# Optimization experiments

Hardware: AMD Instinct MI355X
Metric: run time of the kernel (lower is better)

The kernel has to match this reference:

```python
import jax, jax.numpy as jnp
import numpy as np

N_QUBITS = 4
N_LAYERS = 2
BATCH = 2097152  # 2**21

# All gates (RY, CNOT) are real-valued and the initial state |0..0> is real,
# so the whole simulation stays in float32; <Z> is then real automatically
# (matching the .real taken in the torch module).

def _apply_ry(state, theta, q):
    """Apply RY(theta) on qubit q. state: (B,2,2,2,2); theta: scalar or (B,)."""
    s = jnp.moveaxis(state, 1 + q, -1)           # qubit axis -> last
    half = theta * 0.5
    c, sn = jnp.cos(half), jnp.sin(half)
    a, bamp = s[..., 0], s[..., 1]               # (B,2,2,2)
    # broadcast per-sample angles over remaining qubit axes
    c = jnp.reshape(c, c.shape + (1,) * (a.ndim - c.ndim))
    sn = jnp.reshape(sn, sn.shape + (1,) * (a.ndim - sn.ndim))
    new = jnp.stack([c * a - sn * bamp, sn * a + c * bamp], axis=-1)
    return jnp.moveaxis(new, -1, 1 + q)


def _apply_cnot(state, ctrl, tgt):
    """CNOT(ctrl -> tgt). Swap target amplitudes where control bit is 1."""
    s = jnp.moveaxis(state, (1 + ctrl, 1 + tgt), (-2, -1))
    s = jnp.stack([s[..., 0, :], s[..., 1, ::-1]], axis=-2)
    return jnp.moveaxis(s, (-2, -1), (1 + ctrl, 1 + tgt))


def _circuit(x, weights):
    """x: (B, n_qubits) angles; weights: (n_layers, n_qubits). Returns (B, n_qubits) <Z_i>."""
    B = x.shape[0]
    state = jnp.zeros((B,) + (2,) * N_QUBITS, dtype=x.dtype)
    state = state.at[(slice(None),) + (0,) * N_QUBITS].set(1.0)  # |0000>
    for i in range(N_QUBITS):
        state = _apply_ry(state, x[:, i], i)
    for l in range(N_LAYERS):
        for i in range(N_QUBITS):
            state = _apply_cnot(state, i, (i + 1) % N_QUBITS)
        for i in range(N_QUBITS):
            state = _apply_ry(state, weights[l, i], i)
    p = state * state                             # probabilities (real state)
    zs = []
    for i in range(N_QUBITS):
        pm = jnp.moveaxis(p, 1 + i, -1)
        zs.append((pm[..., 0] - pm[..., 1]).sum(axis=(1, 2, 3)))
    return jnp.stack(zs, axis=-1)


def setup_inputs() -> dict:
    key = jax.random.key(0)
    k1, k2, k3, k4 = jax.random.split(key, 4)
    return {
        "x": jax.random.normal(k1, (BATCH, N_QUBITS), dtype=jnp.float32),
        "weights": jax.random.normal(k2, (N_LAYERS, N_QUBITS), dtype=jnp.float32),
        "W": jax.random.normal(k3, (2, N_QUBITS), dtype=jnp.float32) / np.sqrt(N_QUBITS),
        "b": jax.random.normal(k4, (2,), dtype=jnp.float32) * 0.01,
    }


def reference(x, weights, W, b):
    features = _circuit(x, weights)               # (B, 4)
    return features @ W.T + b                     # (B, 2)
```

## Files before the change

### kernel.cpp

```cpp
#include <hip/hip_runtime.h>


template<int BIT>
__device__ __forceinline__ void apply_ry(float (&a)[16], float c, float s) {
#pragma unroll
    for (int i = 0; i < 16; ++i) {
        if ((i & BIT) == 0) {
            float a0 = a[i];
            float a1 = a[i | BIT];
            a[i]       = __builtin_fmaf(c, a0, -(s * a1));
            a[i | BIT] = __builtin_fmaf(s, a0,  (c * a1));
        }
    }
}

template<int CBIT, int TBIT>
__device__ __forceinline__ void apply_cnot(float (&a)[16]) {
#pragma unroll
    for (int i = 0; i < 16; ++i) {
        if ((i & CBIT) != 0 && (i & TBIT) == 0) {
            float t = a[i];
            a[i] = a[i | TBIT];
            a[i | TBIT] = t;
        }
    }
}

__global__ __launch_bounds__(256) void qsim_kernel(
    const float4* __restrict__ x4,
    const float*  __restrict__ wts,
    const float*  __restrict__ W,
    const float*  __restrict__ bias,
    float2*       __restrict__ out,
    int B)
{
    int i = blockIdx.x * blockDim.x + threadIdx.x;
    if (i >= B) return;

    float4 xa = x4[i];

    float c0, s0, c1, s1, c2, s2, c3, s3;
    __sincosf(0.5f * xa.x, &s0, &c0);
    __sincosf(0.5f * xa.y, &s1, &c1);
    __sincosf(0.5f * xa.z, &s2, &c2);
    __sincosf(0.5f * xa.w, &s3, &c3);

    float cw[8], sw[8];
#pragma unroll
    for (int k = 0; k < 8; ++k) {
        __sincosf(0.5f * wts[k], &sw[k], &cw[k]);
    }

    float a[16];
    {
        float p00 = c0 * c1, p01 = c0 * s1, p10 = s0 * c1, p11 = s0 * s1;
        float q00 = c2 * c3, q01 = c2 * s3, q10 = s2 * c3, q11 = s2 * s3;
        a[ 0] = p00 * q00; a[ 1] = p00 * q01; a[ 2] = p00 * q10; a[ 3] = p00 * q11;
        a[ 4] = p01 * q00; a[ 5] = p01 * q01; a[ 6] = p01 * q10; a[ 7] = p01 * q11;
        a[ 8] = p10 * q00; a[ 9] = p10 * q01; a[10] = p10 * q10; a[11] = p10 * q11;
        a[12] = p11 * q00; a[13] = p11 * q01; a[14] = p11 * q10; a[15] = p11 * q11;
    }

#pragma unroll
    for (int l = 0; l < 2; ++l) {
        apply_cnot<8, 4>(a);
        apply_cnot<4, 2>(a);
        apply_cnot<2, 1>(a);
        apply_cnot<1, 8>(a);
        apply_ry<8>(a, cw[l * 4 + 0], sw[l * 4 + 0]);
        apply_ry<4>(a, cw[l * 4 + 1], sw[l * 4 + 1]);
        apply_ry<2>(a, cw[l * 4 + 2], sw[l * 4 + 2]);
        apply_ry<1>(a, cw[l * 4 + 3], sw[l * 4 + 3]);
    }

    float z0 = 0.f, z1 = 0.f, z2 = 0.f, z3 = 0.f;
#pragma unroll
    for (int s = 0; s < 16; ++s) {
        float p = a[s] * a[s];
        z0 += (s & 8) ? -p : p;
        z1 += (s & 4) ? -p : p;
        z2 += (s & 2) ? -p : p;
        z3 += (s & 1) ? -p : p;
    }

    float o0 = bias[0];
    o0 = __builtin_fmaf(z0, W[0], o0);
    o0 = __builtin_fmaf(z1, W[1], o0);
    o0 = __builtin_fmaf(z2, W[2], o0);
    o0 = __builtin_fmaf(z3, W[3], o0);
    float o1 = bias[1];
    o1 = __builtin_fmaf(z0, W[4], o1);
    o1 = __builtin_fmaf(z1, W[5], o1);
    o1 = __builtin_fmaf(z2, W[6], o1);
    o1 = __builtin_fmaf(z3, W[7], o1);

    out[i] = make_float2(o0, o1);
}

extern "C" void kernel_launch(void* const* d_in, const int* in_sizes, int n_in,
                              void* d_out, int out_size, void* d_ws, size_t ws_size,
                              hipStream_t stream) {
    const float* x    = (const float*)d_in[0];
    const float* wts  = (const float*)d_in[1];
    const float* W    = (const float*)d_in[2];
    const float* bias = (const float*)d_in[3];
    float* out = (float*)d_out;

    int B = in_sizes[0] / 4;
    int block = 256;
    int grid = (B + block - 1) / block;
    qsim_kernel<<<grid, block, 0, stream>>>(
        (const float4*)x, wts, W, bias, (float2*)out, B);
}
```

Before: 98.85 us.

## Fold final RY layer into Z expectation algebra and use nontemporal IO

Drops the last layer of RY gates from the simulation. Their effect on each <Z_q> is computed analytically as cos(w)*<Z> - 2*sin(w)*<cross term>, and cos/sin are folded into the linear-layer weights up front. The Z sums are rebuilt with a butterfly of partial sums, and the cross terms come from FMA dot products. The input load and output store also become nontemporal. The aim is fewer ALU ops per sample, but since the kernel is largely memory-bound over 2M samples, the gain may be small.

```diff
diff --git a/kernel.cpp b/kernel.cpp
--- a/kernel.cpp
+++ b/kernel.cpp
@@ -1,5 +1,7 @@
 #include <hip/hip_runtime.h>
 
+typedef float vfloat4 __attribute__((ext_vector_type(4)));
+typedef float vfloat2 __attribute__((ext_vector_type(2)));
 
 template<int BIT>
 __device__ __forceinline__ void apply_ry(float (&a)[16], float c, float s) {
@@ -27,29 +29,39 @@
 }
 
 __global__ __launch_bounds__(256) void qsim_kernel(
-    const float4* __restrict__ x4,
+    const vfloat4* __restrict__ x4,
     const float*  __restrict__ wts,
     const float*  __restrict__ W,
     const float*  __restrict__ bias,
-    float2*       __restrict__ out,
+    vfloat2*      __restrict__ out,
     int B)
 {
     int i = blockIdx.x * blockDim.x + threadIdx.x;
     if (i >= B) return;
 
-    float4 xa = x4[i];
+    float cw[4], sw[4];
+#pragma unroll
+    for (int q = 0; q < 4; ++q) {
+        __sincosf(0.5f * wts[q], &sw[q], &cw[q]);
+    }
+    float wc0[4], wc1[4], wsn0[4], wsn1[4];
+#pragma unroll
+    for (int q = 0; q < 4; ++q) {
+        float S, C;
+        __sincosf(wts[4 + q], &S, &C);
+        wc0[q]  = W[q]     * C;
+        wc1[q]  = W[4 + q] * C;
+        wsn0[q] = -2.0f * W[q]     * S;
+        wsn1[q] = -2.0f * W[4 + q] * S;
+    }
+    float b0 = bias[0], b1 = bias[1];
 
+    vfloat4 xa = __builtin_nontemporal_load(&x4[i]);
     float c0, s0, c1, s1, c2, s2, c3, s3;
     __sincosf(0.5f * xa.x, &s0, &c0);
     __sincosf(0.5f * xa.y, &s1, &c1);
     __sincosf(0.5f * xa.z, &s2, &c2);
     __sincosf(0.5f * xa.w, &s3, &c3);
-
-    float cw[8], sw[8];
-#pragma unroll
-    for (int k = 0; k < 8; ++k) {
-        __sincosf(0.5f * wts[k], &sw[k], &cw[k]);
-    }
 
     float a[16];
     {
@@ -61,40 +73,89 @@
         a[12] = p11 * q00; a[13] = p11 * q01; a[14] = p11 * q10; a[15] = p11 * q11;
     }
 
+    apply_cnot<8, 4>(a);
+    apply_cnot<4, 2>(a);
+    apply_cnot<2, 1>(a);
+    apply_cnot<1, 8>(a);
+    apply_ry<8>(a, cw[0], sw[0]);
+    apply_ry<4>(a, cw[1], sw[1]);
+    apply_ry<2>(a, cw[2], sw[2]);
+    apply_ry<1>(a, cw[3], sw[3]);
+
+    apply_cnot<8, 4>(a);
+    apply_cnot<4, 2>(a);
+    apply_cnot<2, 1>(a);
+    apply_cnot<1, 8>(a);
+
+    float p[16];
 #pragma unroll
-    for (int l = 0; l < 2; ++l) {
-        apply_cnot<8, 4>(a);
-        apply_cnot<4, 2>(a);
-        apply_cnot<2, 1>(a);
-        apply_cnot<1, 8>(a);
-        apply_ry<8>(a, cw[l * 4 + 0], sw[l * 4 + 0]);
-        apply_ry<4>(a, cw[l * 4 + 1], sw[l * 4 + 1]);
-        apply_ry<2>(a, cw[l * 4 + 2], sw[l * 4 + 2]);
-        apply_ry<1>(a, cw[l * 4 + 3], sw[l * 4 + 3]);
-    }
+    for (int s = 0; s < 16; ++s) p[s] = a[s] * a[s];
 
-    float z0 = 0.f, z1 = 0.f, z2 = 0.f, z3 = 0.f;
+    float A[8], D[8];
 #pragma unroll
-    for (int s = 0; s < 16; ++s) {
-        float p = a[s] * a[s];
-        z0 += (s & 8) ? -p : p;
-        z1 += (s & 4) ? -p : p;
-        z2 += (s & 2) ? -p : p;
-        z3 += (s & 1) ? -p : p;
-    }
+    for (int t = 0; t < 8; ++t) { A[t] = p[t] + p[t + 8]; D[t] = p[t] - p[t + 8]; }
+    float dz0 = ((D[0] + D[1]) + (D[2] + D[3])) + ((D[4] + D[5]) + (D[6] + D[7]));
 
-    float o0 = bias[0];
-    o0 = __builtin_fmaf(z0, W[0], o0);
-    o0 = __builtin_fmaf(z1, W[1], o0);
-    o0 = __builtin_fmaf(z2, W[2], o0);
-    o0 = __builtin_fmaf(z3, W[3], o0);
-    float o1 = bias[1];
-    o1 = __builtin_fmaf(z0, W[4], o1);
-    o1 = __builtin_fmaf(z1, W[5], o1);
-    o1 = __builtin_fmaf(z2, W[6], o1);
-    o1 = __builtin_fmaf(z3, W[7], o1);
+    float A2[4], D2[4];
+#pragma unroll
+    for (int t = 0; t < 4; ++t) { A2[t] = A[t] + A[t + 4]; D2[t] = A[t] - A[t + 4]; }
+    float dz1 = (D2[0] + D2[1]) + (D2[2] + D2[3]);
+    float dz2 = (A2[0] - A2[2]) + (A2[1] - A2[3]);
+    float dz3 = (A2[0] + A2[2]) - (A2[1] + A2[3]);
 
-    out[i] = make_float2(o0, o1);
+    float xz0 = a[0] * a[8];
+#pragma unroll
+    for (int t = 1; t < 8; ++t) xz0 = __builtin_fmaf(a[t], a[t + 8], xz0);
+
+    float xz1 = a[0] * a[4];
+    xz1 = __builtin_fmaf(a[1], a[5], xz1);
+    xz1 = __builtin_fmaf(a[2], a[6], xz1);
+    xz1 = __builtin_fmaf(a[3], a[7], xz1);
+    xz1 = __builtin_fmaf(a[8], a[12], xz1);
+    xz1 = __builtin_fmaf(a[9], a[13], xz1);
+    xz1 = __builtin_fmaf(a[10], a[14], xz1);
+    xz1 = __builtin_fmaf(a[11], a[15], xz1);
+
+    float xz2 = a[0] * a[2];
+    xz2 = __builtin_fmaf(a[1],  a[3],  xz2);
+    xz2 = __builtin_fmaf(a[4],  a[6],  xz2);
+    xz2 = __builtin_fmaf(a[5],  a[7],  xz2);
+    xz2 = __builtin_fmaf(a[8],  a[10], xz2);
+    xz2 = __builtin_fmaf(a[9],  a[11], xz2);
+    xz2 = __builtin_fmaf(a[12], a[14], xz2);
+    xz2 = __builtin_fmaf(a[13], a[15], xz2);
+
+    float xz3 = a[0] * a[1];
+    xz3 = __builtin_fmaf(a[2],  a[3],  xz3);
+    xz3 = __builtin_fmaf(a[4],  a[5],  xz3);
+    xz3 = __builtin_fmaf(a[6],  a[7],  xz3);
+    xz3 = __builtin_fmaf(a[8],  a[9],  xz3);
+    xz3 = __builtin_fmaf(a[10], a[11], xz3);
+    xz3 = __builtin_fmaf(a[12], a[13], xz3);
+    xz3 = __builtin_fmaf(a[14], a[15], xz3);
+
+    float o0 = b0;
+    o0 = __builtin_fmaf(wc0[0], dz0, o0);
+    o0 = __builtin_fmaf(wc0[1], dz1, o0);
+    o0 = __builtin_fmaf(wc0[2], dz2, o0);
+    o0 = __builtin_fmaf(wc0[3], dz3, o0);
+    o0 = __builtin_fmaf(wsn0[0], xz0, o0);
+    o0 = __builtin_fmaf(wsn0[1], xz1, o0);
+    o0 = __builtin_fmaf(wsn0[2], xz2, o0);
+    o0 = __builtin_fmaf(wsn0[3], xz3, o0);
+
+    float o1 = b1;
+    o1 = __builtin_fmaf(wc1[0], dz0, o1);
+    o1 = __builtin_fmaf(wc1[1], dz1, o1);
+    o1 = __builtin_fmaf(wc1[2], dz2, o1);
+    o1 = __builtin_fmaf(wc1[3], dz3, o1);
+    o1 = __builtin_fmaf(wsn1[0], xz0, o1);
+    o1 = __builtin_fmaf(wsn1[1], xz1, o1);
+    o1 = __builtin_fmaf(wsn1[2], xz2, o1);
+    o1 = __builtin_fmaf(wsn1[3], xz3, o1);
+
+    vfloat2 o; o.x = o0; o.y = o1;
+    __builtin_nontemporal_store(o, &out[i]);
 }
 
 extern "C" void kernel_launch(void* const* d_in, const int* in_sizes, int n_in,
@@ -110,5 +171,5 @@
     int block = 256;
     int grid = (B + block - 1) / block;
     qsim_kernel<<<grid, block, 0, stream>>>(
-        (const float4*)x, wts, W, bias, (float2*)out, B);
+        (const vfloat4*)x, wts, W, bias, (vfloat2*)out, B);
 }
```

Result: faster. 96.22 us (-2.7%).

## Fold final RY layer into expectation algebra and process two samples per thread

Applied to the files above, without the earlier changes.

The final layer of RY gates is removed analytically: each <Z_q> after RY(w) is rewritten as cos(w)·<Z> − 2·sin(w)·<X-like cross term> on the pre-rotation state, and these factors are folded into precomputed per-qubit weights combined with the linear head. Each thread now handles two samples using packed 2-wide float vectors, so the compiler can emit packed FMA/mul instructions. Loads and stores use nontemporal 16-byte accesses, and the Z sums are built with a butterfly add tree. Together these cut per-sample ALU work and halve the thread count. The cost is higher register pressure, and an odd batch size would leave the last sample unprocessed.

```diff
diff --git a/kernel.cpp b/kernel.cpp
--- a/kernel.cpp
+++ b/kernel.cpp
@@ -1,25 +1,30 @@
 #include <hip/hip_runtime.h>
 
 
+typedef float v2 __attribute__((ext_vector_type(2)));
+typedef float vfloat4 __attribute__((ext_vector_type(4)));
+
+#define FMA2(A, B, C) __builtin_elementwise_fma((v2)(A), (v2)(B), (v2)(C))
+
 template<int BIT>
-__device__ __forceinline__ void apply_ry(float (&a)[16], float c, float s) {
+__device__ __forceinline__ void apply_ry(v2 (&a)[16], float c, float s) {
 #pragma unroll
     for (int i = 0; i < 16; ++i) {
         if ((i & BIT) == 0) {
-            float a0 = a[i];
-            float a1 = a[i | BIT];
-            a[i]       = __builtin_fmaf(c, a0, -(s * a1));
-            a[i | BIT] = __builtin_fmaf(s, a0,  (c * a1));
+            v2 a0 = a[i];
+            v2 a1 = a[i | BIT];
+            a[i]       = FMA2(c, a0, -(s * a1));
+            a[i | BIT] = FMA2(s, a0,  (c * a1));
         }
     }
 }
 
 template<int CBIT, int TBIT>
-__device__ __forceinline__ void apply_cnot(float (&a)[16]) {
+__device__ __forceinline__ void apply_cnot(v2 (&a)[16]) {
 #pragma unroll
     for (int i = 0; i < 16; ++i) {
         if ((i & CBIT) != 0 && (i & TBIT) == 0) {
-            float t = a[i];
+            v2 t = a[i];
             a[i] = a[i | TBIT];
             a[i | TBIT] = t;
         }
@@ -27,74 +32,140 @@
 }
 
 __global__ __launch_bounds__(256) void qsim_kernel(
-    const float4* __restrict__ x4,
+    const vfloat4* __restrict__ x4,
     const float*  __restrict__ wts,
     const float*  __restrict__ W,
     const float*  __restrict__ bias,
-    float2*       __restrict__ out,
-    int B)
+    vfloat4*      __restrict__ out4,
+    int Bhalf)
 {
     int i = blockIdx.x * blockDim.x + threadIdx.x;
-    if (i >= B) return;
+    if (i >= Bhalf) return;
 
-    float4 xa = x4[i];
+    float cw[4], sw[4];
+#pragma unroll
+    for (int q = 0; q < 4; ++q) {
+        __sincosf(0.5f * wts[q], &sw[q], &cw[q]);
+    }
+    float wc0[4], wc1[4], wsn0[4], wsn1[4];
+#pragma unroll
+    for (int q = 0; q < 4; ++q) {
+        float S, C;
+        __sincosf(wts[4 + q], &S, &C);
+        wc0[q]  = W[q]     * C;
+        wc1[q]  = W[4 + q] * C;
+        wsn0[q] = -2.0f * W[q]     * S;
+        wsn1[q] = -2.0f * W[4 + q] * S;
+    }
+    float b0 = bias[0], b1 = bias[1];
 
-    float c0, s0, c1, s1, c2, s2, c3, s3;
-    __sincosf(0.5f * xa.x, &s0, &c0);
-    __sincosf(0.5f * xa.y, &s1, &c1);
-    __sincosf(0.5f * xa.z, &s2, &c2);
-    __sincosf(0.5f * xa.w, &s3, &c3);
+    vfloat4 xA = __builtin_nontemporal_load(&x4[2 * i]);
+    vfloat4 xB = __builtin_nontemporal_load(&x4[2 * i + 1]);
 
-    float cw[8], sw[8];
+    v2 c[4], s[4];
 #pragma unroll
-    for (int k = 0; k < 8; ++k) {
-        __sincosf(0.5f * wts[k], &sw[k], &cw[k]);
+    for (int q = 0; q < 4; ++q) {
+        float sa, ca, sb, cb;
+        __sincosf(0.5f * xA[q], &sa, &ca);
+        __sincosf(0.5f * xB[q], &sb, &cb);
+        c[q].x = ca; c[q].y = cb;
+        s[q].x = sa; s[q].y = sb;
     }
 
-    float a[16];
+    v2 a[16];
     {
-        float p00 = c0 * c1, p01 = c0 * s1, p10 = s0 * c1, p11 = s0 * s1;
-        float q00 = c2 * c3, q01 = c2 * s3, q10 = s2 * c3, q11 = s2 * s3;
+        v2 p00 = c[0] * c[1], p01 = c[0] * s[1], p10 = s[0] * c[1], p11 = s[0] * s[1];
+        v2 q00 = c[2] * c[3], q01 = c[2] * s[3], q10 = s[2] * c[3], q11 = s[2] * s[3];
         a[ 0] = p00 * q00; a[ 1] = p00 * q01; a[ 2] = p00 * q10; a[ 3] = p00 * q11;
         a[ 4] = p01 * q00; a[ 5] = p01 * q01; a[ 6] = p01 * q10; a[ 7] = p01 * q11;
         a[ 8] = p10 * q00; a[ 9] = p10 * q01; a[10] = p10 * q10; a[11] = p10 * q11;
         a[12] = p11 * q00; a[13] = p11 * q01; a[14] = p11 * q10; a[15] = p11 * q11;
     }
 
+    apply_cnot<8, 4>(a);
+    apply_cnot<4, 2>(a);
+    apply_cnot<2, 1>(a);
+    apply_cnot<1, 8>(a);
+    apply_ry<8>(a, cw[0], sw[0]);
+    apply_ry<4>(a, cw[1], sw[1]);
+    apply_ry<2>(a, cw[2], sw[2]);
+    apply_ry<1>(a, cw[3], sw[3]);
+
+    apply_cnot<8, 4>(a);
+    apply_cnot<4, 2>(a);
+    apply_cnot<2, 1>(a);
+    apply_cnot<1, 8>(a);
+
+    v2 xz0 = a[0] * a[8];
 #pragma unroll
-    for (int l = 0; l < 2; ++l) {
-        apply_cnot<8, 4>(a);
-        apply_cnot<4, 2>(a);
-        apply_cnot<2, 1>(a);
-        apply_cnot<1, 8>(a);
-        apply_ry<8>(a, cw[l * 4 + 0], sw[l * 4 + 0]);
-        apply_ry<4>(a, cw[l * 4 + 1], sw[l * 4 + 1]);
-        apply_ry<2>(a, cw[l * 4 + 2], sw[l * 4 + 2]);
-        apply_ry<1>(a, cw[l * 4 + 3], sw[l * 4 + 3]);
-    }
+    for (int t = 1; t < 8; ++t) xz0 = FMA2(a[t], a[t + 8], xz0);
 
-    float z0 = 0.f, z1 = 0.f, z2 = 0.f, z3 = 0.f;
+    v2 xz1 = a[0] * a[4];
+    xz1 = FMA2(a[1], a[5], xz1);
+    xz1 = FMA2(a[2], a[6], xz1);
+    xz1 = FMA2(a[3], a[7], xz1);
+    xz1 = FMA2(a[8], a[12], xz1);
+    xz1 = FMA2(a[9], a[13], xz1);
+    xz1 = FMA2(a[10], a[14], xz1);
+    xz1 = FMA2(a[11], a[15], xz1);
+
+    v2 xz2 = a[0] * a[2];
+    xz2 = FMA2(a[1],  a[3],  xz2);
+    xz2 = FMA2(a[4],  a[6],  xz2);
+    xz2 = FMA2(a[5],  a[7],  xz2);
+    xz2 = FMA2(a[8],  a[10], xz2);
+    xz2 = FMA2(a[9],  a[11], xz2);
+    xz2 = FMA2(a[12], a[14], xz2);
+    xz2 = FMA2(a[13], a[15], xz2);
+
+    v2 xz3 = a[0] * a[1];
+    xz3 = FMA2(a[2],  a[3],  xz3);
+    xz3 = FMA2(a[4],  a[5],  xz3);
+    xz3 = FMA2(a[6],  a[7],  xz3);
+    xz3 = FMA2(a[8],  a[9],  xz3);
+    xz3 = FMA2(a[10], a[11], xz3);
+    xz3 = FMA2(a[12], a[13], xz3);
+    xz3 = FMA2(a[14], a[15], xz3);
+
+    v2 p[16];
 #pragma unroll
-    for (int s = 0; s < 16; ++s) {
-        float p = a[s] * a[s];
-        z0 += (s & 8) ? -p : p;
-        z1 += (s & 4) ? -p : p;
-        z2 += (s & 2) ? -p : p;
-        z3 += (s & 1) ? -p : p;
-    }
+    for (int t = 0; t < 16; ++t) p[t] = a[t] * a[t];
 
-    float o0 = bias[0];
-    o0 = __builtin_fmaf(z0, W[0], o0);
-    o0 = __builtin_fmaf(z1, W[1], o0);
-    o0 = __builtin_fmaf(z2, W[2], o0);
-    o0 = __builtin_fmaf(z3, W[3], o0);
-    float o1 = bias[1];
-    o1 = __builtin_fmaf(z0, W[4], o1);
-    o1 = __builtin_fmaf(z1, W[5], o1);
-    o1 = __builtin_fmaf(z2, W[6], o1);
-    o1 = __builtin_fmaf(z3, W[7], o1);
+    v2 A[8], D[8];
+#pragma unroll
+    for (int t = 0; t < 8; ++t) { A[t] = p[t] + p[t + 8]; D[t] = p[t] - p[t + 8]; }
+    v2 dz0 = ((D[0] + D[1]) + (D[2] + D[3])) + ((D[4] + D[5]) + (D[6] + D[7]));
 
-    out[i] = make_float2(o0, o1);
+    v2 A2[4], D2[4];
+#pragma unroll
+    for (int t = 0; t < 4; ++t) { A2[t] = A[t] + A[t + 4]; D2[t] = A[t] - A[t + 4]; }
+    v2 dz1 = (D2[0] + D2[1]) + (D2[2] + D2[3]);
+    v2 dz2 = (A2[0] - A2[2]) + (A2[1] - A2[3]);
+    v2 dz3 = (A2[0] + A2[2]) - (A2[1] + A2[3]);
+
+    v2 o0 = (v2)(b0);
+    o0 = FMA2(wc0[0], dz0, o0);
+    o0 = FMA2(wc0[1], dz1, o0);
+    o0 = FMA2(wc0[2], dz2, o0);
+    o0 = FMA2(wc0[3], dz3, o0);
+    o0 = FMA2(wsn0[0], xz0, o0);
+    o0 = FMA2(wsn0[1], xz1, o0);
+    o0 = FMA2(wsn0[2], xz2, o0);
+    o0 = FMA2(wsn0[3], xz3, o0);
+
+    v2 o1 = (v2)(b1);
+    o1 = FMA2(wc1[0], dz0, o1);
+    o1 = FMA2(wc1[1], dz1, o1);
+    o1 = FMA2(wc1[2], dz2, o1);
+    o1 = FMA2(wc1[3], dz3, o1);
+    o1 = FMA2(wsn1[0], xz0, o1);
+    o1 = FMA2(wsn1[1], xz1, o1);
+    o1 = FMA2(wsn1[2], xz2, o1);
+    o1 = FMA2(wsn1[3], xz3, o1);
+
+    vfloat4 o;
+    o.x = o0.x; o.y = o1.x; o.z = o0.y; o.w = o1.y;
+    __builtin_nontemporal_store(o, &out4[i]);
 }
 
 extern "C" void kernel_launch(void* const* d_in, const int* in_sizes, int n_in,
@@ -107,8 +178,9 @@
     float* out = (float*)d_out;
 
     int B = in_sizes[0] / 4;
+    int Bhalf = B / 2;
     int block = 256;
-    int grid = (B + block - 1) / block;
+    int grid = (Bhalf + block - 1) / block;
     qsim_kernel<<<grid, block, 0, stream>>>(
-        (const float4*)x, wts, W, bias, (float2*)out, B);
+        (const vfloat4*)x, wts, W, bias, (vfloat4*)out, Bhalf);
 }
```

Result: faster. 93.76 us (-5.1%).
